# Optimization experiments

Hardware: AMD Instinct MI355X
Metric: run time of the kernel (lower is better)

The kernel has to match this reference:

```python
import jax, jax.numpy as jnp
import numpy as np

N_NODES = 50000


def _gcn_conv(x, W, b, src, dst, norm, n_nodes):
    # x: [N, Fin], W: [Fin, Fout]
    h = x @ W                                   # [N, Fout]
    msg = h[src] * norm[:, None]                # [E+N, Fout] edge messages
    out = jax.ops.segment_sum(msg, dst, num_segments=n_nodes)
    return out + b


def reference(x, edge_index, W1, b1, W2, b2):
    n = x.shape[0]
    # add self-loops (PyG GCNConv default add_self_loops=True)
    loop = jnp.arange(n, dtype=edge_index.dtype)
    src = jnp.concatenate([edge_index[0], loop])
    dst = jnp.concatenate([edge_index[1], loop])
    # symmetric degree normalization: deg over destination with unit weights
    deg = jax.ops.segment_sum(jnp.ones_like(dst, dtype=x.dtype), dst, num_segments=n)
    dinv = jnp.where(deg > 0, jax.lax.rsqrt(deg), 0.0)
    norm = dinv[src] * dinv[dst]                # [E+N]
    h = _gcn_conv(x, W1, b1, src, dst, norm, n)
    h = jax.nn.relu(h)
    out = _gcn_conv(h, W2, b2, src, dst, norm, n)
    return out


def setup_inputs() -> dict:
    key = jax.random.key(0)
    k1, k2, k3, k4 = jax.random.split(key, 4)
    n, e, fin, hid, fout = N_NODES, 800000, 128, 128, 64
    x = jax.random.normal(k1, (n, fin), dtype=jnp.float32)
    edge_index = jax.random.randint(k2, (2, e), 0, n, dtype=jnp.int64)
    # Glorot-ish init for linear weights, zero bias (PyG default)
    W1 = jax.random.normal(k3, (fin, hid), dtype=jnp.float32) / np.sqrt(fin)
    b1 = jnp.zeros((hid,), dtype=jnp.float32)
    W2 = jax.random.normal(k4, (hid, fout), dtype=jnp.float32) / np.sqrt(hid)
    b2 = jnp.zeros((fout,), dtype=jnp.float32)
    return {"x": x, "edge_index": edge_index, "W1": W1, "b1": b1, "W2": W2, "b2": b2}
```

## Files before the change

kernel.cpp:

```cpp
#include <hip/hip_runtime.h>
#include <hip/hip_bf16.h>


constexpr int FIN = 128;
constexpr int HID = 128;
constexpr int FOUT = 64;
constexpr int CAP = 48;
constexpr int NPB = 98;
constexpr int BCAP = 3072;
constexpr int OVF_MAX = 65536;

typedef __attribute__((ext_vector_type(8))) short s16x8;
typedef __attribute__((ext_vector_type(4))) float f32x4;

static __device__ __forceinline__ float bf2f(__hip_bfloat16 v) { return __bfloat162float(v); }
static __device__ __forceinline__ float lo2f(unsigned u) { union { unsigned i; float f; } c; c.i = u << 16; return c.f; }
static __device__ __forceinline__ float hi2f(unsigned u) { union { unsigned i; float f; } c; c.i = u & 0xffff0000u; return c.f; }
static __device__ __forceinline__ unsigned short f2bfu(float f) {
    __hip_bfloat16 h = __float2bfloat16(f);
    union { __hip_bfloat16 h; unsigned short u; } c; c.h = h; return c.u;
}
static __device__ __forceinline__ unsigned pack2(float a, float b) {
    return (unsigned)f2bfu(a) | ((unsigned)f2bfu(b) << 16);
}
static __device__ __forceinline__ void acc_add(float* acc, uint4 v) {
    acc[0] += lo2f(v.x); acc[1] += hi2f(v.x);
    acc[2] += lo2f(v.y); acc[3] += hi2f(v.y);
    acc[4] += lo2f(v.z); acc[5] += hi2f(v.z);
    acc[6] += lo2f(v.w); acc[7] += hi2f(v.w);
}
static __device__ __forceinline__ void acc_fma(float* acc, uint4 v, float w) {
    acc[0] += w * lo2f(v.x); acc[1] += w * hi2f(v.x);
    acc[2] += w * lo2f(v.y); acc[3] += w * hi2f(v.y);
    acc[4] += w * lo2f(v.z); acc[5] += w * hi2f(v.z);
    acc[6] += w * lo2f(v.w); acc[7] += w * hi2f(v.w);
}

__global__ __launch_bounds__(256) void k_detect(const unsigned* __restrict__ xw,
                                                const int* __restrict__ eiw,
                                                int E, int* __restrict__ flags,
                                                int* __restrict__ gcur,
                                                int* __restrict__ cnt, int N, int zero_cnt) {
    if (zero_cnt)
        for (long i = (long)blockIdx.x * 256 + threadIdx.x; i < N; i += (long)gridDim.x * 256)
            cnt[i] = 0;
    if (blockIdx.x != 0) return;
    for (int i = threadIdx.x; i < 514; i += 256) gcur[i] = 0;
    __shared__ int s_bf16like, s_oddnz;
    if (threadIdx.x == 0) { s_bf16like = 0; s_oddnz = 0; }
    __syncthreads();
    int c = 0;
    for (int i = threadIdx.x; i < 4096; i += 256) {
        unsigned ex = ((xw[i] & 0xffffu) >> 7) & 0xffu;
        if (ex >= 117u && ex <= 130u) c++;
    }
    atomicAdd(&s_bf16like, c);
    int nz = 0;
    for (int i = threadIdx.x; i < 2048; i += 256)
        if (eiw[2 * i + 1] != 0) nz++;
    atomicAdd(&s_oddnz, nz);
    __syncthreads();
    if (threadIdx.x == 0) {
        flags[0] = (s_bf16like < 2048) ? 1 : 0;
        flags[1] = (s_oddnz == 0) ? 1 : 0;
    }
}

__global__ __launch_bounds__(256) void k_mega(const void* __restrict__ Xp,
                                              const void* __restrict__ Wp,
                                              const int* __restrict__ ei, int E, int N,
                                              int nbuk, int GB,
                                              int* __restrict__ gcur,
                                              unsigned* __restrict__ pairs,
                                              int2* __restrict__ ovfA,
                                              int* __restrict__ ovfAcnt,
                                              __hip_bfloat16* __restrict__ G,
                                              const int* __restrict__ flags) {
    extern __shared__ __align__(16) char smem[];
    const int tid = threadIdx.x;
    if ((int)blockIdx.x < GB) {
        short* Wt = (short*)smem;
        const bool f32m = flags[0] != 0;
        for (int i = tid; i < 128 * 128; i += 256) {
            int k = i >> 7, n = i & 127;
            float wv = f32m ? ((const float*)Wp)[(long)k * 128 + n]
                            : bf2f(((const __hip_bfloat16*)Wp)[(long)k * 128 + n]);
            Wt[n * 136 + k] = (short)f2bfu(wv);
        }
        __syncthreads();
        const int w = tid >> 6, lane = tid & 63;
        const int m = lane & 15, quad = lane >> 4;
        const int rowA = blockIdx.x * 64 + w * 16 + m;
        const int rowc = rowA < N ? rowA : N - 1;
        s16x8 afr[4];
#pragma unroll
        for (int kc = 0; kc < 4; ++kc) {
            const int k0 = kc * 32 + quad * 8;
            if (!f32m) {
                afr[kc] = *(const s16x8*)((const __hip_bfloat16*)Xp + (long)rowc * 128 + k0);
            } else {
                const float* p = (const float*)Xp + (long)rowc * 128 + k0;
                s16x8 t;
#pragma unroll
                for (int j = 0; j < 8; ++j) t[j] = (short)f2bfu(p[j]);
                afr[kc] = t;
            }
        }
        const int rbase = blockIdx.x * 64 + w * 16 + quad * 4;
#pragma unroll
        for (int ct = 0; ct < 8; ++ct) {
            f32x4 acc = {0.f, 0.f, 0.f, 0.f};
#pragma unroll
            for (int kc = 0; kc < 4; ++kc) {
                s16x8 bfr = *(const s16x8*)&Wt[(ct * 16 + m) * 136 + kc * 32 + quad * 8];
                acc = __builtin_amdgcn_mfma_f32_16x16x32_bf16(afr[kc], bfr, acc, 0, 0, 0);
            }
            const int plane = ct >> 2;
            const int cp = (ct & 3) * 16 + m;
#pragma unroll
            for (int r = 0; r < 4; ++r) {
                int rr = rbase + r;
                if (rr < N)
                    G[(long)plane * N * 64 + (long)rr * 64 + cp] = __float2bfloat16(acc[r]);
            }
        }
    } else {
        int* hist = (int*)smem;
        int* gbase = hist + 512;
        const long base = (long)(blockIdx.x - GB) * 2048;
        const bool i64 = flags[1] != 0;
        int se[8], de[8];
        for (int b = tid; b < nbuk; b += 256) hist[b] = 0;
        __syncthreads();
#pragma unroll
        for (int j = 0; j < 8; ++j) {
            long i = base + j * 256 + tid;
            int s = 0, d = -1;
            if (i < E) {
                if (i64) { s = ((const int2*)ei)[i].x; d = ((const int2*)(ei + 2 * (long)E))[i].x; }
                else     { s = ei[i]; d = ei[(long)E + i]; }
                if ((unsigned)s >= (unsigned)N || (unsigned)d >= (unsigned)N) d = -1;
            }
            se[j] = s; de[j] = d;
            if (d >= 0) atomicAdd(&hist[d / NPB], 1);
        }
        __syncthreads();
        for (int b = tid; b < nbuk; b += 256) {
            int h = hist[b];
            gbase[b] = h > 0 ? atomicAdd(&gcur[b], h) : 0;
            hist[b] = 0;
        }
        __syncthreads();
#pragma unroll
        for (int j = 0; j < 8; ++j) {
            int d = de[j];
            if (d < 0) continue;
            int b = d / NPB;
            int p = gbase[b] + atomicAdd(&hist[b], 1);
            if (p < BCAP) {
                pairs[(long)b * BCAP + p] = ((unsigned)(d - b * NPB) << 16) | (unsigned)se[j];
            } else {
                int op = atomicAdd(ovfAcnt, 1);
                if (op < OVF_MAX) ovfA[op] = make_int2(d, se[j]);
            }
        }
    }
}

__global__ __launch_bounds__(256) void k_binB(const int* __restrict__ gcur,
                                              const unsigned* __restrict__ pairs,
                                              const int2* __restrict__ ovfA,
                                              const int* __restrict__ ovfAcnt,
                                              int* __restrict__ cnt,
                                              float* __restrict__ dinv,
                                              unsigned short* __restrict__ slots,
                                              int2* __restrict__ ovf2,
                                              int* __restrict__ ovf2cnt, int N) {
    __shared__ int cntL[NPB];
    __shared__ __align__(16) unsigned short slotsL[NPB * CAP];
    const int b = blockIdx.x;
    const int tid = threadIdx.x;
    const int d0 = b * NPB;
    const int nd = min(NPB, N - d0);
    if (nd <= 0) return;
    for (int i = tid; i < NPB; i += 256) cntL[i] = 0;
    __syncthreads();
    const int c = min(gcur[b], BCAP);
    const unsigned* pb = pairs + (long)b * BCAP;
    for (int i = tid; i < c; i += 256) {
        unsigned p = pb[i];
        int ld = p >> 16;
        int pos = atomicAdd(&cntL[ld], 1);
        if (pos < CAP) {
            slotsL[ld * CAP + pos] = (unsigned short)(p & 0xffffu);
        } else {
            int op = atomicAdd(ovf2cnt, 1);
            if (op < OVF_MAX) ovf2[op] = make_int2(d0 + ld, (int)(p & 0xffffu));
        }
    }
    int na = *ovfAcnt; na = na < OVF_MAX ? na : OVF_MAX;
    for (int i = tid; i < na; i += 256) {
        int2 p = ovfA[i];
        int ld = p.x - d0;
        if ((unsigned)ld < (unsigned)nd) {
            int pos = atomicAdd(&cntL[ld], 1);
            if (pos < CAP) {
                slotsL[ld * CAP + pos] = (unsigned short)p.y;
            } else {
                int op = atomicAdd(ovf2cnt, 1);
                if (op < OVF_MAX) ovf2[op] = p;
            }
        }
    }
    __syncthreads();
    for (int i = tid; i < nd; i += 256) {
        cnt[d0 + i] = cntL[i];
        dinv[d0 + i] = rsqrtf((float)(cntL[i] + 1));
    }
    const uint4* sv = (const uint4*)slotsL;
    uint4* gv = (uint4*)(slots + (long)d0 * CAP);
    const int total8 = (nd * CAP) >> 3;
    for (int i = tid; i < total8; i += 256) gv[i] = sv[i];
}

__global__ __launch_bounds__(256) void k_build_direct(const int* __restrict__ ei, int E, int N,
                                                      int* __restrict__ cnt,
                                                      int* __restrict__ slots,
                                                      int2* __restrict__ ovf2,
                                                      int* __restrict__ ovf2cnt,
                                                      const int* __restrict__ flags) {
    long i = (long)blockIdx.x * 256 + threadIdx.x;
    if (i >= E) return;
    int s, d;
    if (flags[1]) { s = ((const int2*)ei)[i].x; d = ((const int2*)(ei + 2 * (long)E))[i].x; }
    else          { s = ei[i]; d = ei[(long)E + i]; }
    if ((unsigned)s >= (unsigned)N || (unsigned)d >= (unsigned)N) return;
    int pos = atomicAdd(&cnt[d], 1);
    if (pos < CAP) {
        slots[(long)d * CAP + pos] = s;
    } else {
        int op = atomicAdd(ovf2cnt, 1);
        if (op < OVF_MAX) ovf2[op] = make_int2(d, s);
    }
}

template<int CT, int SPLIT>
__global__ __launch_bounds__(256) void k_gemm(const void* __restrict__ Xp, int x_follows_flag,
                                              const void* __restrict__ Wp,
                                              const int* __restrict__ cnt,
                                              __hip_bfloat16* __restrict__ G,
                                              const int* __restrict__ flags, int N) {
    constexpr int C = CT * 16;
    __shared__ __align__(16) short Wt[C * 136];
    const bool f32m = flags[0] != 0;
    const bool xf32 = (x_follows_flag != 0) && f32m;
    const int tid = threadIdx.x;
    for (int i = tid; i < 128 * C; i += 256) {
        int k = i / C, n = i % C;
        float wv = f32m ? ((const float*)Wp)[(long)k * C + n]
                        : bf2f(((const __hip_bfloat16*)Wp)[(long)k * C + n]);
        Wt[n * 136 + k] = (short)f2bfu(wv);
    }
    __syncthreads();
    const int w = tid >> 6, lane = tid & 63;
    const int m = lane & 15, quad = lane >> 4;
    const int rowA = blockIdx.x * 64 + w * 16 + m;
    const int rowc = rowA < N ? rowA : N - 1;
    s16x8 afr[4];
#pragma unroll
    for (int kc = 0; kc < 4; ++kc) {
        const int k0 = kc * 32 + quad * 8;
        if (!xf32) {
            afr[kc] = *(const s16x8*)((const __hip_bfloat16*)Xp + (long)rowc * 128 + k0);
        } else {
            const float* p = (const float*)Xp + (long)rowc * 128 + k0;
            s16x8 t;
#pragma unroll
            for (int j = 0; j < 8; ++j) t[j] = (short)f2bfu(p[j]);
            afr[kc] = t;
        }
    }
    const int rbase = blockIdx.x * 64 + w * 16 + quad * 4;
    float dv[4];
#pragma unroll
    for (int r = 0; r < 4; ++r) {
        int rr = min(rbase + r, N - 1);
        dv[r] = rsqrtf((float)(cnt[rr] + 1));
    }
#pragma unroll
    for (int ct = 0; ct < CT; ++ct) {
        f32x4 acc = {0.f, 0.f, 0.f, 0.f};
#pragma unroll
        for (int kc = 0; kc < 4; ++kc) {
            s16x8 bfr = *(const s16x8*)&Wt[(ct * 16 + m) * 136 + kc * 32 + quad * 8];
            acc = __builtin_amdgcn_mfma_f32_16x16x32_bf16(afr[kc], bfr, acc, 0, 0, 0);
        }
#pragma unroll
        for (int r = 0; r < 4; ++r) {
            int rr = rbase + r;
            if (rr < N) {
                long off;
                if (SPLIT) {
                    const int plane = ct / (CT / 2);
                    const int cp = (ct % (CT / 2)) * 16 + m;
                    off = (long)plane * N * (C / 2) + (long)rr * (C / 2) + cp;
                } else {
                    off = (long)rr * C + ct * 16 + m;
                }
                G[off] = __float2bfloat16(dv[r] * acc[r]);
            }
        }
    }
}

__global__ __launch_bounds__(256) void k_gather1(const __hip_bfloat16* __restrict__ G,
                                                 const int* __restrict__ cnt,
                                                 const float* __restrict__ dinv,
                                                 const unsigned short* __restrict__ slots,
                                                 const int2* __restrict__ ovf2,
                                                 const int* __restrict__ ovf2cnt,
                                                 const void* __restrict__ b1,
                                                 __hip_bfloat16* __restrict__ h1,
                                                 const int* __restrict__ flags, int N) {
    const int half = gridDim.x >> 1;
    int bx = blockIdx.x;
    const int P = bx >= half ? 1 : 0;
    if (P) bx -= half;
    const __hip_bfloat16* Gp = G + (long)P * N * 64;
    const int tid = threadIdx.x;
    const int grp = tid >> 3, lane = tid & 7;
    const int node = bx * 32 + grp;
    if (node >= N) return;
    const int cd = cnt[node];
    const float wself = dinv[node];
    const int m = cd < CAP ? cd : CAP;
    const unsigned short* sl = slots + (long)node * CAP;
    float acc[8] = {0, 0, 0, 0, 0, 0, 0, 0};
    acc_fma(acc, ((const uint4*)(Gp + (long)node * 64))[lane], wself);
    int i = 0;
    for (; i + 7 < m; i += 8) {
        int s0 = sl[i], s1 = sl[i + 1], s2 = sl[i + 2], s3 = sl[i + 3];
        int s4 = sl[i + 4], s5 = sl[i + 5], s6 = sl[i + 6], s7 = sl[i + 7];
        float w0 = dinv[s0], w1 = dinv[s1], w2 = dinv[s2], w3 = dinv[s3];
        float w4 = dinv[s4], w5 = dinv[s5], w6 = dinv[s6], w7 = dinv[s7];
        uint4 v0 = ((const uint4*)(Gp + (long)s0 * 64))[lane];
        uint4 v1 = ((const uint4*)(Gp + (long)s1 * 64))[lane];
        uint4 v2 = ((const uint4*)(Gp + (long)s2 * 64))[lane];
        uint4 v3 = ((const uint4*)(Gp + (long)s3 * 64))[lane];
        uint4 v4 = ((const uint4*)(Gp + (long)s4 * 64))[lane];
        uint4 v5 = ((const uint4*)(Gp + (long)s5 * 64))[lane];
        uint4 v6 = ((const uint4*)(Gp + (long)s6 * 64))[lane];
        uint4 v7 = ((const uint4*)(Gp + (long)s7 * 64))[lane];
        acc_fma(acc, v0, w0); acc_fma(acc, v1, w1); acc_fma(acc, v2, w2); acc_fma(acc, v3, w3);
        acc_fma(acc, v4, w4); acc_fma(acc, v5, w5); acc_fma(acc, v6, w6); acc_fma(acc, v7, w7);
    }
    for (; i + 3 < m; i += 4) {
        int s0 = sl[i], s1 = sl[i + 1], s2 = sl[i + 2], s3 = sl[i + 3];
        float w0 = dinv[s0], w1 = dinv[s1], w2 = dinv[s2], w3 = dinv[s3];
        uint4 v0 = ((const uint4*)(Gp + (long)s0 * 64))[lane];
        uint4 v1 = ((const uint4*)(Gp + (long)s1 * 64))[lane];
        uint4 v2 = ((const uint4*)(Gp + (long)s2 * 64))[lane];
        uint4 v3 = ((const uint4*)(Gp + (long)s3 * 64))[lane];
        acc_fma(acc, v0, w0); acc_fma(acc, v1, w1); acc_fma(acc, v2, w2); acc_fma(acc, v3, w3);
    }
    for (; i < m; ++i) {
        int s0 = sl[i];
        acc_fma(acc, ((const uint4*)(Gp + (long)s0 * 64))[lane], dinv[s0]);
    }
    if (cd > CAP) {
        int oc = *ovf2cnt; oc = oc < OVF_MAX ? oc : OVF_MAX;
        for (int j = 0; j < oc; ++j)
            if (ovf2[j].x == node) {
                int s0 = ovf2[j].y;
                acc_fma(acc, ((const uint4*)(Gp + (long)s0 * 64))[lane], dinv[s0]);
            }
    }
    const bool f32m = flags[0] != 0;
    const int c0 = P * 64 + lane * 8;
    float bv[8];
    if (f32m) {
        const float4* bp = (const float4*)((const float*)b1 + c0);
        float4 b0 = bp[0], b1v = bp[1];
        bv[0] = b0.x; bv[1] = b0.y; bv[2] = b0.z; bv[3] = b0.w;
        bv[4] = b1v.x; bv[5] = b1v.y; bv[6] = b1v.z; bv[7] = b1v.w;
    } else {
        uint4 b = *(const uint4*)((const __hip_bfloat16*)b1 + c0);
        bv[0] = lo2f(b.x); bv[1] = hi2f(b.x); bv[2] = lo2f(b.y); bv[3] = hi2f(b.y);
        bv[4] = lo2f(b.z); bv[5] = hi2f(b.z); bv[6] = lo2f(b.w); bv[7] = hi2f(b.w);
    }
    float o[8];
#pragma unroll
    for (int c = 0; c < 8; ++c) {
        float v = wself * acc[c] + bv[c];
        o[c] = v > 0.f ? v : 0.f;
    }
    uint4 pv = { pack2(o[0], o[1]), pack2(o[2], o[3]), pack2(o[4], o[5]), pack2(o[6], o[7]) };
    ((uint4*)(h1 + (long)node * 128 + P * 64))[lane] = pv;
}

template<int F, int LAYER1, typename ST>
__global__ __launch_bounds__(256) void k_gather(const __hip_bfloat16* __restrict__ G,
                                                const int* __restrict__ cnt,
                                                const ST* __restrict__ slots,
                                                const int2* __restrict__ ovf2,
                                                const int* __restrict__ ovf2cnt,
                                                const void* __restrict__ bias,
                                                void* __restrict__ outp,
                                                const int* __restrict__ flags, int N) {
    constexpr int L = F / 8;
    constexpr int NODES = 256 / L;
    const int tid = threadIdx.x;
    const int grp = tid / L, lane = tid % L;
    const int node = blockIdx.x * NODES + grp;
    if (node >= N) return;
    const int cd = cnt[node];
    const float wself = rsqrtf((float)(cd + 1));
    const int m = cd < CAP ? cd : CAP;
    const ST* sl = slots + (long)node * CAP;
    float acc[8] = {0, 0, 0, 0, 0, 0, 0, 0};
    acc_add(acc, ((const uint4*)(G + (long)node * F))[lane]);
    int i = 0;
    for (; i + 7 < m; i += 8) {
        int s0 = sl[i], s1 = sl[i + 1], s2 = sl[i + 2], s3 = sl[i + 3];
        int s4 = sl[i + 4], s5 = sl[i + 5], s6 = sl[i + 6], s7 = sl[i + 7];
        uint4 v0 = ((const uint4*)(G + (long)s0 * F))[lane];
        uint4 v1 = ((const uint4*)(G + (long)s1 * F))[lane];
        uint4 v2 = ((const uint4*)(G + (long)s2 * F))[lane];
        uint4 v3 = ((const uint4*)(G + (long)s3 * F))[lane];
        uint4 v4 = ((const uint4*)(G + (long)s4 * F))[lane];
        uint4 v5 = ((const uint4*)(G + (long)s5 * F))[lane];
        uint4 v6 = ((const uint4*)(G + (long)s6 * F))[lane];
        uint4 v7 = ((const uint4*)(G + (long)s7 * F))[lane];
        acc_add(acc, v0); acc_add(acc, v1); acc_add(acc, v2); acc_add(acc, v3);
        acc_add(acc, v4); acc_add(acc, v5); acc_add(acc, v6); acc_add(acc, v7);
    }
    for (; i + 3 < m; i += 4) {
        int s0 = sl[i], s1 = sl[i + 1], s2 = sl[i + 2], s3 = sl[i + 3];
        uint4 v0 = ((const uint4*)(G + (long)s0 * F))[lane];
        uint4 v1 = ((const uint4*)(G + (long)s1 * F))[lane];
        uint4 v2 = ((const uint4*)(G + (long)s2 * F))[lane];
        uint4 v3 = ((const uint4*)(G + (long)s3 * F))[lane];
        acc_add(acc, v0); acc_add(acc, v1); acc_add(acc, v2); acc_add(acc, v3);
    }
    for (; i < m; ++i)
        acc_add(acc, ((const uint4*)(G + (long)sl[i] * F))[lane]);
    if (cd > CAP) {
        int oc = *ovf2cnt; oc = oc < OVF_MAX ? oc : OVF_MAX;
        for (int j = 0; j < oc; ++j)
            if (ovf2[j].x == node)
                acc_add(acc, ((const uint4*)(G + (long)ovf2[j].y * F))[lane]);
    }
    const bool f32m = flags[0] != 0;
    const int c0 = lane * 8;
    float bv[8];
    if (f32m) {
        const float4* bp = (const float4*)((const float*)bias + c0);
        float4 b0 = bp[0], b1 = bp[1];
        bv[0] = b0.x; bv[1] = b0.y; bv[2] = b0.z; bv[3] = b0.w;
        bv[4] = b1.x; bv[5] = b1.y; bv[6] = b1.z; bv[7] = b1.w;
    } else {
        uint4 b = *(const uint4*)((const __hip_bfloat16*)bias + c0);
        bv[0] = lo2f(b.x); bv[1] = hi2f(b.x); bv[2] = lo2f(b.y); bv[3] = hi2f(b.y);
        bv[4] = lo2f(b.z); bv[5] = hi2f(b.z); bv[6] = lo2f(b.w); bv[7] = hi2f(b.w);
    }
    float o[8];
#pragma unroll
    for (int c = 0; c < 8; ++c) {
        float v = wself * acc[c] + bv[c];
        o[c] = (LAYER1 && v < 0.f) ? 0.f : v;
    }
    if (LAYER1 || !f32m) {
        uint4 pv = { pack2(o[0], o[1]), pack2(o[2], o[3]), pack2(o[4], o[5]), pack2(o[6], o[7]) };
        ((uint4*)outp)[(long)node * L + lane] = pv;
    } else {
        float4* op = (float4*)((float*)outp + (long)node * F + c0);
        op[0] = make_float4(o[0], o[1], o[2], o[3]);
        op[1] = make_float4(o[4], o[5], o[6], o[7]);
    }
}

extern "C" void kernel_launch(void* const* d_in, const int* in_sizes, int n_in,
                              void* d_out, int out_size, void* d_ws, size_t ws_size,
                              hipStream_t stream) {
    const void* x  = d_in[0];
    const int*  ei = (const int*)d_in[1];
    const void* W1 = d_in[2];
    const void* b1 = d_in[3];
    const void* W2 = d_in[4];
    const void* b2 = d_in[5];

    const int N = in_sizes[0] / FIN;
    const int E = in_sizes[1] / 2;
    const int nbuk = (N + NPB - 1) / NPB;

    char* ws = (char*)d_ws;
    int*   flags   = (int*)ws;
    int*   gcur    = (int*)(ws + 4096);
    int*   ovfAcnt = gcur + 512;
    int*   ovf2cnt = gcur + 513;
    int*   cnt     = (int*)(ws + 65536);
    float* dinv    = (float*)(ws + 266240);
    int2*  ovfA    = (int2*)(ws + 524288);
    int2*  ovf2    = (int2*)(ws + 1048576);
    unsigned short* slots16 = (unsigned short*)(ws + 2097152);
    int*   slots32 = (int*)(ws + 2097152);
    __hip_bfloat16* g  = (__hip_bfloat16*)(ws + 11730944);
    __hip_bfloat16* g2 = g;
    unsigned* pairs = (unsigned*)(ws + 24530944);
    __hip_bfloat16* h1 = (__hip_bfloat16*)(ws + 24530944);

    const int GB = (N + 63) / 64;
    const int AB = (E + 2047) / 2048;
    const int EB = (E + 255) / 256;

    if (N <= 65536 && nbuk <= 512) {
        k_detect<<<1, 256, 0, stream>>>((const unsigned*)x, ei, E, flags, gcur, cnt, N, 0);
        k_mega<<<GB + AB, 256, 34816, stream>>>(x, W1, ei, E, N, nbuk, GB,
                                                gcur, pairs, ovfA, ovfAcnt, g, flags);
        k_binB<<<nbuk, 256, 0, stream>>>(gcur, pairs, ovfA, ovfAcnt, cnt, dinv, slots16, ovf2, ovf2cnt, N);
        const int half = (N + 31) / 32;
        k_gather1<<<2 * half, 256, 0, stream>>>(g, cnt, dinv, slots16, ovf2, ovf2cnt, b1, h1, flags, N);
        k_gemm<4, 0><<<GB, 256, 0, stream>>>(h1, 0, W2, cnt, g2, flags, N);
        k_gather<64, 0, unsigned short><<<(N + 31) / 32, 256, 0, stream>>>(
            g2, cnt, slots16, ovf2, ovf2cnt, b2, d_out, flags, N);
    } else {
        k_detect<<<64, 256, 0, stream>>>((const unsigned*)x, ei, E, flags, gcur, cnt, N, 1);
        k_build_direct<<<EB, 256, 0, stream>>>(ei, E, N, cnt, slots32, ovf2, ovf2cnt, flags);
        k_gemm<8, 0><<<GB, 256, 0, stream>>>(x, 1, W1, cnt, g, flags, N);
        k_gather<128, 1, int><<<(N + 15) / 16, 256, 0, stream>>>(
            g, cnt, slots32, ovf2, ovf2cnt, b1, h1, flags, N);
        k_gemm<4, 0><<<GB, 256, 0, stream>>>(h1, 0, W2, cnt, g2, flags, N);
        k_gather<64, 0, int><<<(N + 31) / 32, 256, 0, stream>>>(
            g2, cnt, slots32, ovf2, ovf2cnt, b2, d_out, flags, N);
    }
}
```

Before: 190.7 us.

## Split feature planes into 32-column slabs and stage neighbor lists in LDS

```diff
diff --git a/kernel.cpp b/kernel.cpp
--- a/kernel.cpp
+++ b/kernel.cpp
@@ -35,6 +35,8 @@
     acc[4] += w * lo2f(v.z); acc[5] += w * hi2f(v.z);
     acc[6] += w * lo2f(v.w); acc[7] += w * hi2f(v.w);
 }
+
+struct SW { int s; float w; };
 
 __global__ __launch_bounds__(256) void k_detect(const unsigned* __restrict__ xw,
                                                 const int* __restrict__ eiw,
@@ -115,13 +117,13 @@
                 s16x8 bfr = *(const s16x8*)&Wt[(ct * 16 + m) * 136 + kc * 32 + quad * 8];
                 acc = __builtin_amdgcn_mfma_f32_16x16x32_bf16(afr[kc], bfr, acc, 0, 0, 0);
             }
-            const int plane = ct >> 2;
-            const int cp = (ct & 3) * 16 + m;
+            const int plane = ct >> 1;
+            const int cp = (ct & 1) * 16 + m;
 #pragma unroll
             for (int r = 0; r < 4; ++r) {
                 int rr = rbase + r;
                 if (rr < N)
-                    G[(long)plane * N * 64 + (long)rr * 64 + cp] = __float2bfloat16(acc[r]);
+                    G[(long)plane * N * 32 + (long)rr * 32 + cp] = __float2bfloat16(acc[r]);
             }
         }
     } else {
@@ -313,89 +315,206 @@
     }
 }
 
-__global__ __launch_bounds__(256) void k_gather1(const __hip_bfloat16* __restrict__ G,
-                                                 const int* __restrict__ cnt,
-                                                 const float* __restrict__ dinv,
-                                                 const unsigned short* __restrict__ slots,
-                                                 const int2* __restrict__ ovf2,
-                                                 const int* __restrict__ ovf2cnt,
-                                                 const void* __restrict__ b1,
-                                                 __hip_bfloat16* __restrict__ h1,
-                                                 const int* __restrict__ flags, int N) {
-    const int half = gridDim.x >> 1;
-    int bx = blockIdx.x;
-    const int P = bx >= half ? 1 : 0;
-    if (P) bx -= half;
-    const __hip_bfloat16* Gp = G + (long)P * N * 64;
+__global__ __launch_bounds__(256) void k_gather1p(const __hip_bfloat16* __restrict__ G,
+                                                  const int* __restrict__ cnt,
+                                                  const float* __restrict__ dinv,
+                                                  const unsigned short* __restrict__ slots,
+                                                  const int2* __restrict__ ovf2,
+                                                  const int* __restrict__ ovf2cnt,
+                                                  const void* __restrict__ b1,
+                                                  __hip_bfloat16* __restrict__ h1,
+                                                  const int* __restrict__ flags, int N) {
+    __shared__ int cntL[64];
+    __shared__ float wsL[64];
+    __shared__ __align__(16) SW swL[64 * 49];
     const int tid = threadIdx.x;
-    const int grp = tid >> 3, lane = tid & 7;
-    const int node = bx * 32 + grp;
-    if (node >= N) return;
-    const int cd = cnt[node];
-    const float wself = dinv[node];
+    const int n0 = blockIdx.x * 64;
+    const int nd = min(64, N - n0);
+    for (int i = tid; i < nd; i += 256) {
+        cntL[i] = cnt[n0 + i];
+        wsL[i] = dinv[n0 + i];
+    }
+    __syncthreads();
+    for (int j = tid; j < 64 * CAP; j += 256) {
+        const int ni = j / CAP, sl = j - ni * CAP;
+        if (ni < nd) {
+            const int mm = min(cntL[ni], CAP);
+            if (sl < mm) {
+                const int s = slots[(long)(n0 + ni) * CAP + sl];
+                swL[ni * 49 + sl].s = s;
+                swL[ni * 49 + sl].w = dinv[s];
+            }
+        }
+    }
+    __syncthreads();
+    const int grp = tid >> 2, lane = tid & 3;
+    if (grp >= nd) return;
+    const int node = n0 + grp;
+    const int cd = cntL[grp];
     const int m = cd < CAP ? cd : CAP;
-    const unsigned short* sl = slots + (long)node * CAP;
-    float acc[8] = {0, 0, 0, 0, 0, 0, 0, 0};
-    acc_fma(acc, ((const uint4*)(Gp + (long)node * 64))[lane], wself);
-    int i = 0;
-    for (; i + 7 < m; i += 8) {
-        int s0 = sl[i], s1 = sl[i + 1], s2 = sl[i + 2], s3 = sl[i + 3];
-        int s4 = sl[i + 4], s5 = sl[i + 5], s6 = sl[i + 6], s7 = sl[i + 7];
-        float w0 = dinv[s0], w1 = dinv[s1], w2 = dinv[s2], w3 = dinv[s3];
-        float w4 = dinv[s4], w5 = dinv[s5], w6 = dinv[s6], w7 = dinv[s7];
-        uint4 v0 = ((const uint4*)(Gp + (long)s0 * 64))[lane];
-        uint4 v1 = ((const uint4*)(Gp + (long)s1 * 64))[lane];
-        uint4 v2 = ((const uint4*)(Gp + (long)s2 * 64))[lane];
-        uint4 v3 = ((const uint4*)(Gp + (long)s3 * 64))[lane];
-        uint4 v4 = ((const uint4*)(Gp + (long)s4 * 64))[lane];
-        uint4 v5 = ((const uint4*)(Gp + (long)s5 * 64))[lane];
-        uint4 v6 = ((const uint4*)(Gp + (long)s6 * 64))[lane];
-        uint4 v7 = ((const uint4*)(Gp + (long)s7 * 64))[lane];
-        acc_fma(acc, v0, w0); acc_fma(acc, v1, w1); acc_fma(acc, v2, w2); acc_fma(acc, v3, w3);
-        acc_fma(acc, v4, w4); acc_fma(acc, v5, w5); acc_fma(acc, v6, w6); acc_fma(acc, v7, w7);
-    }
-    for (; i + 3 < m; i += 4) {
-        int s0 = sl[i], s1 = sl[i + 1], s2 = sl[i + 2], s3 = sl[i + 3];
-        float w0 = dinv[s0], w1 = dinv[s1], w2 = dinv[s2], w3 = dinv[s3];
-        uint4 v0 = ((const uint4*)(Gp + (long)s0 * 64))[lane];
-        uint4 v1 = ((const uint4*)(Gp + (long)s1 * 64))[lane];
-        uint4 v2 = ((const uint4*)(Gp + (long)s2 * 64))[lane];
-        uint4 v3 = ((const uint4*)(Gp + (long)s3 * 64))[lane];
-        acc_fma(acc, v0, w0); acc_fma(acc, v1, w1); acc_fma(acc, v2, w2); acc_fma(acc, v3, w3);
-    }
-    for (; i < m; ++i) {
-        int s0 = sl[i];
-        acc_fma(acc, ((const uint4*)(Gp + (long)s0 * 64))[lane], dinv[s0]);
-    }
-    if (cd > CAP) {
-        int oc = *ovf2cnt; oc = oc < OVF_MAX ? oc : OVF_MAX;
-        for (int j = 0; j < oc; ++j)
-            if (ovf2[j].x == node) {
-                int s0 = ovf2[j].y;
-                acc_fma(acc, ((const uint4*)(Gp + (long)s0 * 64))[lane], dinv[s0]);
-            }
-    }
+    const float wself = wsL[grp];
+    const SW* sw = &swL[grp * 49];
     const bool f32m = flags[0] != 0;
-    const int c0 = P * 64 + lane * 8;
-    float bv[8];
-    if (f32m) {
-        const float4* bp = (const float4*)((const float*)b1 + c0);
-        float4 b0 = bp[0], b1v = bp[1];
-        bv[0] = b0.x; bv[1] = b0.y; bv[2] = b0.z; bv[3] = b0.w;
-        bv[4] = b1v.x; bv[5] = b1v.y; bv[6] = b1v.z; bv[7] = b1v.w;
-    } else {
-        uint4 b = *(const uint4*)((const __hip_bfloat16*)b1 + c0);
-        bv[0] = lo2f(b.x); bv[1] = hi2f(b.x); bv[2] = lo2f(b.y); bv[3] = hi2f(b.y);
-        bv[4] = lo2f(b.z); bv[5] = hi2f(b.z); bv[6] = lo2f(b.w); bv[7] = hi2f(b.w);
-    }
-    float o[8];
-#pragma unroll
-    for (int c = 0; c < 8; ++c) {
-        float v = wself * acc[c] + bv[c];
-        o[c] = v > 0.f ? v : 0.f;
-    }
-    uint4 pv = { pack2(o[0], o[1]), pack2(o[2], o[3]), pack2(o[4], o[5]), pack2(o[6], o[7]) };
-    ((uint4*)(h1 + (long)node * 128 + P * 64))[lane] = pv;
+    for (int P = 0; P < 4; ++P) {
+        const __hip_bfloat16* Gp = G + (long)P * N * 32;
+        float acc[8] = {0, 0, 0, 0, 0, 0, 0, 0};
+        acc_fma(acc, ((const uint4*)(Gp + (long)node * 32))[lane], wself);
+        int i = 0;
+        for (; i + 7 < m; i += 8) {
+            SW a0 = sw[i], a1 = sw[i + 1], a2 = sw[i + 2], a3 = sw[i + 3];
+            SW a4 = sw[i + 4], a5 = sw[i + 5], a6 = sw[i + 6], a7 = sw[i + 7];
+            uint4 v0 = ((const uint4*)(Gp + (long)a0.s * 32))[lane];
+            uint4 v1 = ((const uint4*)(Gp + (long)a1.s * 32))[lane];
+            uint4 v2 = ((const uint4*)(Gp + (long)a2.s * 32))[lane];
+            uint4 v3 = ((const uint4*)(Gp + (long)a3.s * 32))[lane];
+            uint4 v4 = ((const uint4*)(Gp + (long)a4.s * 32))[lane];
+            uint4 v5 = ((const uint4*)(Gp + (long)a5.s * 32))[lane];
+            uint4 v6 = ((const uint4*)(Gp + (long)a6.s * 32))[lane];
+            uint4 v7 = ((const uint4*)(Gp + (long)a7.s * 32))[lane];
+            acc_fma(acc, v0, a0.w); acc_fma(acc, v1, a1.w);
+            acc_fma(acc, v2, a2.w); acc_fma(acc, v3, a3.w);
+            acc_fma(acc, v4, a4.w); acc_fma(acc, v5, a5.w);
+            acc_fma(acc, v6, a6.w); acc_fma(acc, v7, a7.w);
+        }
+        for (; i + 3 < m; i += 4) {
+            SW a0 = sw[i], a1 = sw[i + 1], a2 = sw[i + 2], a3 = sw[i + 3];
+            uint4 v0 = ((const uint4*)(Gp + (long)a0.s * 32))[lane];
+            uint4 v1 = ((const uint4*)(Gp + (long)a1.s * 32))[lane];
+            uint4 v2 = ((const uint4*)(Gp + (long)a2.s * 32))[lane];
+            uint4 v3 = ((const uint4*)(Gp + (long)a3.s * 32))[lane];
+            acc_fma(acc, v0, a0.w); acc_fma(acc, v1, a1.w);
+            acc_fma(acc, v2, a2.w); acc_fma(acc, v3, a3.w);
+        }
+        for (; i < m; ++i) {
+            SW a = sw[i];
+            acc_fma(acc, ((const uint4*)(Gp + (long)a.s * 32))[lane], a.w);
+        }
+        if (cd > CAP) {
+            int oc = *ovf2cnt; oc = oc < OVF_MAX ? oc : OVF_MAX;
+            for (int j = 0; j < oc; ++j)
+                if (ovf2[j].x == node) {
+                    int s0 = ovf2[j].y;
+                    acc_fma(acc, ((const uint4*)(Gp + (long)s0 * 32))[lane], dinv[s0]);
+                }
+        }
+        const int c0 = P * 32 + lane * 8;
+        float bv[8];
+        if (f32m) {
+            const float4* bp = (const float4*)((const float*)b1 + c0);
+            float4 b0 = bp[0], b1v = bp[1];
+            bv[0] = b0.x; bv[1] = b0.y; bv[2] = b0.z; bv[3] = b0.w;
+            bv[4] = b1v.x; bv[5] = b1v.y; bv[6] = b1v.z; bv[7] = b1v.w;
+        } else {
+            uint4 b = *(const uint4*)((const __hip_bfloat16*)b1 + c0);
+            bv[0] = lo2f(b.x); bv[1] = hi2f(b.x); bv[2] = lo2f(b.y); bv[3] = hi2f(b.y);
+            bv[4] = lo2f(b.z); bv[5] = hi2f(b.z); bv[6] = lo2f(b.w); bv[7] = hi2f(b.w);
+        }
+        float o[8];
+#pragma unroll
+        for (int c = 0; c < 8; ++c) {
+            float v = wself * acc[c] + bv[c];
+            o[c] = v > 0.f ? v : 0.f;
+        }
+        uint4 pv = { pack2(o[0], o[1]), pack2(o[2], o[3]), pack2(o[4], o[5]), pack2(o[6], o[7]) };
+        ((uint4*)(h1 + (long)node * 128 + P * 32))[lane] = pv;
+    }
+}
+
+__global__ __launch_bounds__(256) void k_gather2p(const __hip_bfloat16* __restrict__ G,
+                                                  const int* __restrict__ cnt,
+                                                  const float* __restrict__ dinv,
+                                                  const unsigned short* __restrict__ slots,
+                                                  const int2* __restrict__ ovf2,
+                                                  const int* __restrict__ ovf2cnt,
+                                                  const void* __restrict__ bias,
+                                                  void* __restrict__ outp,
+                                                  const int* __restrict__ flags, int N) {
+    __shared__ int cntL[64];
+    __shared__ float wsL[64];
+    __shared__ int slL[64 * 49];
+    const int tid = threadIdx.x;
+    const int n0 = blockIdx.x * 64;
+    const int nd = min(64, N - n0);
+    for (int i = tid; i < nd; i += 256) {
+        cntL[i] = cnt[n0 + i];
+        wsL[i] = dinv[n0 + i];
+    }
+    __syncthreads();
+    for (int j = tid; j < 64 * CAP; j += 256) {
+        const int ni = j / CAP, sl = j - ni * CAP;
+        if (ni < nd) {
+            const int mm = min(cntL[ni], CAP);
+            if (sl < mm) slL[ni * 49 + sl] = slots[(long)(n0 + ni) * CAP + sl];
+        }
+    }
+    __syncthreads();
+    const int grp = tid >> 2, lane = tid & 3;
+    if (grp >= nd) return;
+    const int node = n0 + grp;
+    const int cd = cntL[grp];
+    const int m = cd < CAP ? cd : CAP;
+    const float wself = wsL[grp];
+    const int* sl = &slL[grp * 49];
+    const bool f32m = flags[0] != 0;
+    for (int P = 0; P < 2; ++P) {
+        const __hip_bfloat16* Gp = G + (long)P * N * 32;
+        float acc[8] = {0, 0, 0, 0, 0, 0, 0, 0};
+        acc_add(acc, ((const uint4*)(Gp + (long)node * 32))[lane]);
+        int i = 0;
+        for (; i + 7 < m; i += 8) {
+            int s0 = sl[i], s1 = sl[i + 1], s2 = sl[i + 2], s3 = sl[i + 3];
+            int s4 = sl[i + 4], s5 = sl[i + 5], s6 = sl[i + 6], s7 = sl[i + 7];
+            uint4 v0 = ((const uint4*)(Gp + (long)s0 * 32))[lane];
+            uint4 v1 = ((const uint4*)(Gp + (long)s1 * 32))[lane];
+            uint4 v2 = ((const uint4*)(Gp + (long)s2 * 32))[lane];
+            uint4 v3 = ((const uint4*)(Gp + (long)s3 * 32))[lane];
+            uint4 v4 = ((const uint4*)(Gp + (long)s4 * 32))[lane];
+            uint4 v5 = ((const uint4*)(Gp + (long)s5 * 32))[lane];
+            uint4 v6 = ((const uint4*)(Gp + (long)s6 * 32))[lane];
+            uint4 v7 = ((const uint4*)(Gp + (long)s7 * 32))[lane];
+            acc_add(acc, v0); acc_add(acc, v1); acc_add(acc, v2); acc_add(acc, v3);
+            acc_add(acc, v4); acc_add(acc, v5); acc_add(acc, v6); acc_add(acc, v7);
+        }
+        for (; i + 3 < m; i += 4) {
+            int s0 = sl[i], s1 = sl[i + 1], s2 = sl[i + 2], s3 = sl[i + 3];
+            uint4 v0 = ((const uint4*)(Gp + (long)s0 * 32))[lane];
+            uint4 v1 = ((const uint4*)(Gp + (long)s1 * 32))[lane];
+            uint4 v2 = ((const uint4*)(Gp + (long)s2 * 32))[lane];
+            uint4 v3 = ((const uint4*)(Gp + (long)s3 * 32))[lane];
+            acc_add(acc, v0); acc_add(acc, v1); acc_add(acc, v2); acc_add(acc, v3);
+        }
+        for (; i < m; ++i)
+            acc_add(acc, ((const uint4*)(Gp + (long)sl[i] * 32))[lane]);
+        if (cd > CAP) {
+            int oc = *ovf2cnt; oc = oc < OVF_MAX ? oc : OVF_MAX;
+            for (int j = 0; j < oc; ++j)
+                if (ovf2[j].x == node)
+                    acc_add(acc, ((const uint4*)(Gp + (long)ovf2[j].y * 32))[lane]);
+        }
+        const int c0 = P * 32 + lane * 8;
+        float bv[8];
+        if (f32m) {
+            const float4* bp = (const float4*)((const float*)bias + c0);
+            float4 b0 = bp[0], b1 = bp[1];
+            bv[0] = b0.x; bv[1] = b0.y; bv[2] = b0.z; bv[3] = b0.w;
+            bv[4] = b1.x; bv[5] = b1.y; bv[6] = b1.z; bv[7] = b1.w;
+        } else {
+            uint4 b = *(const uint4*)((const __hip_bfloat16*)bias + c0);
+            bv[0] = lo2f(b.x); bv[1] = hi2f(b.x); bv[2] = lo2f(b.y); bv[3] = hi2f(b.y);
+            bv[4] = lo2f(b.z); bv[5] = hi2f(b.z); bv[6] = lo2f(b.w); bv[7] = hi2f(b.w);
+        }
+        float o[8];
+#pragma unroll
+        for (int c = 0; c < 8; ++c) o[c] = wself * acc[c] + bv[c];
+        if (!f32m) {
+            uint4 pv = { pack2(o[0], o[1]), pack2(o[2], o[3]), pack2(o[4], o[5]), pack2(o[6], o[7]) };
+            ((uint4*)outp)[(long)node * 8 + P * 4 + lane] = pv;
+        } else {
+            float4* op = (float4*)((float*)outp + (long)node * FOUT + c0);
+            op[0] = make_float4(o[0], o[1], o[2], o[3]);
+            op[1] = make_float4(o[4], o[5], o[6], o[7]);
+        }
+    }
 }
 
 template<int F, int LAYER1, typename ST>
@@ -518,11 +637,10 @@
         k_mega<<<GB + AB, 256, 34816, stream>>>(x, W1, ei, E, N, nbuk, GB,
                                                 gcur, pairs, ovfA, ovfAcnt, g, flags);
         k_binB<<<nbuk, 256, 0, stream>>>(gcur, pairs, ovfA, ovfAcnt, cnt, dinv, slots16, ovf2, ovf2cnt, N);
-        const int half = (N + 31) / 32;
-        k_gather1<<<2 * half, 256, 0, stream>>>(g, cnt, dinv, slots16, ovf2, ovf2cnt, b1, h1, flags, N);
-        k_gemm<4, 0><<<GB, 256, 0, stream>>>(h1, 0, W2, cnt, g2, flags, N);
-        k_gather<64, 0, unsigned short><<<(N + 31) / 32, 256, 0, stream>>>(
-            g2, cnt, slots16, ovf2, ovf2cnt, b2, d_out, flags, N);
+        const int GBL = (N + 63) / 64;
+        k_gather1p<<<GBL, 256, 0, stream>>>(g, cnt, dinv, slots16, ovf2, ovf2cnt, b1, h1, flags, N);
+        k_gemm<4, 1><<<GB, 256, 0, stream>>>(h1, 0, W2, cnt, g2, flags, N);
+        k_gather2p<<<GBL, 256, 0, stream>>>(g2, cnt, dinv, slots16, ovf2, ovf2cnt, b2, d_out, flags, N);
     } else {
         k_detect<<<64, 256, 0, stream>>>((const unsigned*)x, ei, E, flags, gcur, cnt, N, 1);
         k_build_direct<<<EB, 256, 0, stream>>>(ei, E, N, cnt, slots32, ovf2, ovf2cnt, flags);
```

New measurement: 199.4 us. 1.05x slower.

## Stage neighbor slots and weights in LDS and process both planes per block

Applied to the files above, without the earlier changes.

```diff
diff --git a/kernel.cpp b/kernel.cpp
--- a/kernel.cpp
+++ b/kernel.cpp
@@ -35,6 +35,8 @@
     acc[4] += w * lo2f(v.z); acc[5] += w * hi2f(v.z);
     acc[6] += w * lo2f(v.w); acc[7] += w * hi2f(v.w);
 }
+
+struct SW { int s; float w; };
 
 __global__ __launch_bounds__(256) void k_detect(const unsigned* __restrict__ xw,
                                                 const int* __restrict__ eiw,
@@ -313,89 +315,109 @@
     }
 }
 
-__global__ __launch_bounds__(256) void k_gather1(const __hip_bfloat16* __restrict__ G,
-                                                 const int* __restrict__ cnt,
-                                                 const float* __restrict__ dinv,
-                                                 const unsigned short* __restrict__ slots,
-                                                 const int2* __restrict__ ovf2,
-                                                 const int* __restrict__ ovf2cnt,
-                                                 const void* __restrict__ b1,
-                                                 __hip_bfloat16* __restrict__ h1,
-                                                 const int* __restrict__ flags, int N) {
-    const int half = gridDim.x >> 1;
-    int bx = blockIdx.x;
-    const int P = bx >= half ? 1 : 0;
-    if (P) bx -= half;
-    const __hip_bfloat16* Gp = G + (long)P * N * 64;
+__global__ __launch_bounds__(256) void k_gather1b(const __hip_bfloat16* __restrict__ G,
+                                                  const int* __restrict__ cnt,
+                                                  const float* __restrict__ dinv,
+                                                  const unsigned short* __restrict__ slots,
+                                                  const int2* __restrict__ ovf2,
+                                                  const int* __restrict__ ovf2cnt,
+                                                  const void* __restrict__ b1,
+                                                  __hip_bfloat16* __restrict__ h1,
+                                                  const int* __restrict__ flags, int N) {
+    __shared__ int cntL[32];
+    __shared__ float wsL[32];
+    __shared__ __align__(16) SW swL[32 * 49];
     const int tid = threadIdx.x;
+    const int n0 = blockIdx.x * 32;
+    const int nd = min(32, N - n0);
+    for (int i = tid; i < nd; i += 256) {
+        cntL[i] = cnt[n0 + i];
+        wsL[i] = dinv[n0 + i];
+    }
+    __syncthreads();
+    for (int j = tid; j < 32 * CAP; j += 256) {
+        const int ni = j / CAP, sl = j - ni * CAP;
+        if (ni < nd) {
+            const int mm = min(cntL[ni], CAP);
+            if (sl < mm) {
+                const int s = slots[(long)(n0 + ni) * CAP + sl];
+                swL[ni * 49 + sl].s = s;
+                swL[ni * 49 + sl].w = dinv[s];
+            }
+        }
+    }
+    __syncthreads();
     const int grp = tid >> 3, lane = tid & 7;
-    const int node = bx * 32 + grp;
-    if (node >= N) return;
-    const int cd = cnt[node];
-    const float wself = dinv[node];
+    if (grp >= nd) return;
+    const int node = n0 + grp;
+    const int cd = cntL[grp];
     const int m = cd < CAP ? cd : CAP;
-    const unsigned short* sl = slots + (long)node * CAP;
-    float acc[8] = {0, 0, 0, 0, 0, 0, 0, 0};
-    acc_fma(acc, ((const uint4*)(Gp + (long)node * 64))[lane], wself);
-    int i = 0;
-    for (; i + 7 < m; i += 8) {
-        int s0 = sl[i], s1 = sl[i + 1], s2 = sl[i + 2], s3 = sl[i + 3];
-        int s4 = sl[i + 4], s5 = sl[i + 5], s6 = sl[i + 6], s7 = sl[i + 7];
-        float w0 = dinv[s0], w1 = dinv[s1], w2 = dinv[s2], w3 = dinv[s3];
-        float w4 = dinv[s4], w5 = dinv[s5], w6 = dinv[s6], w7 = dinv[s7];
-        uint4 v0 = ((const uint4*)(Gp + (long)s0 * 64))[lane];
-        uint4 v1 = ((const uint4*)(Gp + (long)s1 * 64))[lane];
-        uint4 v2 = ((const uint4*)(Gp + (long)s2 * 64))[lane];
-        uint4 v3 = ((const uint4*)(Gp + (long)s3 * 64))[lane];
-        uint4 v4 = ((const uint4*)(Gp + (long)s4 * 64))[lane];
-        uint4 v5 = ((const uint4*)(Gp + (long)s5 * 64))[lane];
-        uint4 v6 = ((const uint4*)(Gp + (long)s6 * 64))[lane];
-        uint4 v7 = ((const uint4*)(Gp + (long)s7 * 64))[lane];
-        acc_fma(acc, v0, w0); acc_fma(acc, v1, w1); acc_fma(acc, v2, w2); acc_fma(acc, v3, w3);
-        acc_fma(acc, v4, w4); acc_fma(acc, v5, w5); acc_fma(acc, v6, w6); acc_fma(acc, v7, w7);
-    }
-    for (; i + 3 < m; i += 4) {
-        int s0 = sl[i], s1 = sl[i + 1], s2 = sl[i + 2], s3 = sl[i + 3];
-        float w0 = dinv[s0], w1 = dinv[s1], w2 = dinv[s2], w3 = dinv[s3];
-        uint4 v0 = ((const uint4*)(Gp + (long)s0 * 64))[lane];
-        uint4 v1 = ((const uint4*)(Gp + (long)s1 * 64))[lane];
-        uint4 v2 = ((const uint4*)(Gp + (long)s2 * 64))[lane];
-        uint4 v3 = ((const uint4*)(Gp + (long)s3 * 64))[lane];
-        acc_fma(acc, v0, w0); acc_fma(acc, v1, w1); acc_fma(acc, v2, w2); acc_fma(acc, v3, w3);
-    }
-    for (; i < m; ++i) {
-        int s0 = sl[i];
-        acc_fma(acc, ((const uint4*)(Gp + (long)s0 * 64))[lane], dinv[s0]);
-    }
-    if (cd > CAP) {
-        int oc = *ovf2cnt; oc = oc < OVF_MAX ? oc : OVF_MAX;
-        for (int j = 0; j < oc; ++j)
-            if (ovf2[j].x == node) {
-                int s0 = ovf2[j].y;
-                acc_fma(acc, ((const uint4*)(Gp + (long)s0 * 64))[lane], dinv[s0]);
-            }
-    }
+    const float wself = wsL[grp];
+    const SW* sw = &swL[grp * 49];
     const bool f32m = flags[0] != 0;
-    const int c0 = P * 64 + lane * 8;
-    float bv[8];
-    if (f32m) {
-        const float4* bp = (const float4*)((const float*)b1 + c0);
-        float4 b0 = bp[0], b1v = bp[1];
-        bv[0] = b0.x; bv[1] = b0.y; bv[2] = b0.z; bv[3] = b0.w;
-        bv[4] = b1v.x; bv[5] = b1v.y; bv[6] = b1v.z; bv[7] = b1v.w;
-    } else {
-        uint4 b = *(const uint4*)((const __hip_bfloat16*)b1 + c0);
-        bv[0] = lo2f(b.x); bv[1] = hi2f(b.x); bv[2] = lo2f(b.y); bv[3] = hi2f(b.y);
-        bv[4] = lo2f(b.z); bv[5] = hi2f(b.z); bv[6] = lo2f(b.w); bv[7] = hi2f(b.w);
-    }
-    float o[8];
-#pragma unroll
-    for (int c = 0; c < 8; ++c) {
-        float v = wself * acc[c] + bv[c];
-        o[c] = v > 0.f ? v : 0.f;
-    }
-    uint4 pv = { pack2(o[0], o[1]), pack2(o[2], o[3]), pack2(o[4], o[5]), pack2(o[6], o[7]) };
-    ((uint4*)(h1 + (long)node * 128 + P * 64))[lane] = pv;
+    for (int P = 0; P < 2; ++P) {
+        const __hip_bfloat16* Gp = G + (long)P * N * 64;
+        float acc[8] = {0, 0, 0, 0, 0, 0, 0, 0};
+        acc_fma(acc, ((const uint4*)(Gp + (long)node * 64))[lane], wself);
+        int i = 0;
+        for (; i + 7 < m; i += 8) {
+            SW a0 = sw[i], a1 = sw[i + 1], a2 = sw[i + 2], a3 = sw[i + 3];
+            SW a4 = sw[i + 4], a5 = sw[i + 5], a6 = sw[i + 6], a7 = sw[i + 7];
+            uint4 v0 = ((const uint4*)(Gp + (long)a0.s * 64))[lane];
+            uint4 v1 = ((const uint4*)(Gp + (long)a1.s * 64))[lane];
+            uint4 v2 = ((const uint4*)(Gp + (long)a2.s * 64))[lane];
+            uint4 v3 = ((const uint4*)(Gp + (long)a3.s * 64))[lane];
+            uint4 v4 = ((const uint4*)(Gp + (long)a4.s * 64))[lane];
+            uint4 v5 = ((const uint4*)(Gp + (long)a5.s * 64))[lane];
+            uint4 v6 = ((const uint4*)(Gp + (long)a6.s * 64))[lane];
+            uint4 v7 = ((const uint4*)(Gp + (long)a7.s * 64))[lane];
+            acc_fma(acc, v0, a0.w); acc_fma(acc, v1, a1.w);
+            acc_fma(acc, v2, a2.w); acc_fma(acc, v3, a3.w);
+            acc_fma(acc, v4, a4.w); acc_fma(acc, v5, a5.w);
+            acc_fma(acc, v6, a6.w); acc_fma(acc, v7, a7.w);
+        }
+        for (; i + 3 < m; i += 4) {
+            SW a0 = sw[i], a1 = sw[i + 1], a2 = sw[i + 2], a3 = sw[i + 3];
+            uint4 v0 = ((const uint4*)(Gp + (long)a0.s * 64))[lane];
+            uint4 v1 = ((const uint4*)(Gp + (long)a1.s * 64))[lane];
+            uint4 v2 = ((const uint4*)(Gp + (long)a2.s * 64))[lane];
+            uint4 v3 = ((const uint4*)(Gp + (long)a3.s * 64))[lane];
+            acc_fma(acc, v0, a0.w); acc_fma(acc, v1, a1.w);
+            acc_fma(acc, v2, a2.w); acc_fma(acc, v3, a3.w);
+        }
+        for (; i < m; ++i) {
+            SW a = sw[i];
+            acc_fma(acc, ((const uint4*)(Gp + (long)a.s * 64))[lane], a.w);
+        }
+        if (cd > CAP) {
+            int oc = *ovf2cnt; oc = oc < OVF_MAX ? oc : OVF_MAX;
+            for (int j = 0; j < oc; ++j)
+                if (ovf2[j].x == node) {
+                    int s0 = ovf2[j].y;
+                    acc_fma(acc, ((const uint4*)(Gp + (long)s0 * 64))[lane], dinv[s0]);
+                }
+        }
+        const int c0 = P * 64 + lane * 8;
+        float bv[8];
+        if (f32m) {
+            const float4* bp = (const float4*)((const float*)b1 + c0);
+            float4 b0 = bp[0], b1v = bp[1];
+            bv[0] = b0.x; bv[1] = b0.y; bv[2] = b0.z; bv[3] = b0.w;
+            bv[4] = b1v.x; bv[5] = b1v.y; bv[6] = b1v.z; bv[7] = b1v.w;
+        } else {
+            uint4 b = *(const uint4*)((const __hip_bfloat16*)b1 + c0);
+            bv[0] = lo2f(b.x); bv[1] = hi2f(b.x); bv[2] = lo2f(b.y); bv[3] = hi2f(b.y);
+            bv[4] = lo2f(b.z); bv[5] = hi2f(b.z); bv[6] = lo2f(b.w); bv[7] = hi2f(b.w);
+        }
+        float o[8];
+#pragma unroll
+        for (int c = 0; c < 8; ++c) {
+            float v = wself * acc[c] + bv[c];
+            o[c] = v > 0.f ? v : 0.f;
+        }
+        uint4 pv = { pack2(o[0], o[1]), pack2(o[2], o[3]), pack2(o[4], o[5]), pack2(o[6], o[7]) };
+        ((uint4*)(h1 + (long)node * 128 + P * 64))[lane] = pv;
+    }
 }
 
 template<int F, int LAYER1, typename ST>
@@ -518,8 +540,8 @@
         k_mega<<<GB + AB, 256, 34816, stream>>>(x, W1, ei, E, N, nbuk, GB,
                                                 gcur, pairs, ovfA, ovfAcnt, g, flags);
         k_binB<<<nbuk, 256, 0, stream>>>(gcur, pairs, ovfA, ovfAcnt, cnt, dinv, slots16, ovf2, ovf2cnt, N);
-        const int half = (N + 31) / 32;
-        k_gather1<<<2 * half, 256, 0, stream>>>(g, cnt, dinv, slots16, ovf2, ovf2cnt, b1, h1, flags, N);
+        const int GBL = (N + 31) / 32;
+        k_gather1b<<<GBL, 256, 0, stream>>>(g, cnt, dinv, slots16, ovf2, ovf2cnt, b1, h1, flags, N);
         k_gemm<4, 0><<<GB, 256, 0, stream>>>(h1, 0, W2, cnt, g2, flags, N);
         k_gather<64, 0, unsigned short><<<(N + 31) / 32, 256, 0, stream>>>(
             g2, cnt, slots16, ovf2, ovf2cnt, b2, d_out, flags, N);
```

After: 190.9 us. Within noise of the previous version (+0.1%).
